# Kernel tuning notes

Measured on AMD Instinct MI355X. Metric: run time of the kernel, lower is better.

## Reference

```python
import jax, jax.numpy as jnp
import numpy as np

B, N, FIN = 512, 256, 32   # batch, num_agents, (tgt_feat+rbt_feat)*2
H1, G, FOUT, K, ACT = 16, 8, 16, 3, 5  # compress dims, shared feat G, GF out, taps, actions


def setup_inputs() -> dict:
    key = jax.random.key(0)
    ks = jax.random.split(key, 10)
    x = jax.random.normal(ks[0], (B, N, FIN), dtype=jnp.float32)
    # GSO, scaled ~1/sqrt(N) so repeated shifts stay numerically tame
    S = jax.random.normal(ks[1], (B, N, N), dtype=jnp.float32) * (1.0 / np.sqrt(N))
    def lin(k, fout, fin):
        return jax.random.normal(k, (fout, fin), dtype=jnp.float32) * (1.0 / np.sqrt(fin))
    W1, b1 = lin(ks[2], H1, FIN), jnp.zeros((H1,), jnp.float32)
    W2, b2 = lin(ks[3], G, H1), jnp.zeros((G,), jnp.float32)
    # graph-filter taps: [FOUT, K, G] (E=1 folded away)
    Hgf = jax.random.normal(ks[4], (FOUT, K, G), dtype=jnp.float32) * (1.0 / np.sqrt(K * G))
    bgf = jnp.zeros((FOUT,), jnp.float32)
    Wa, ba = lin(ks[5], ACT, FOUT), jnp.zeros((ACT,), jnp.float32)
    return {"x": x, "S": S, "W1": W1, "b1": b1, "W2": W2, "b2": b2,
            "Hgf": Hgf, "bgf": bgf, "Wa": Wa, "ba": ba}


def reference(x, S, W1, b1, W2, b2, Hgf, bgf, Wa, ba):
    # compress MLP, batched over all agents at once (replaces the per-agent loop)
    h = jax.nn.relu(jnp.einsum('bnf,hf->bnh', x, W1) + b1)
    h = jax.nn.relu(jnp.einsum('bnh,gh->bng', h, W2) + b2)   # [B, N, G]
    z = jnp.transpose(h, (0, 2, 1))                          # [B, G, N]
    # K-tap graph shift: z_k = z_{k-1} @ S
    taps = [z]
    for _ in range(K - 1):
        taps.append(jnp.einsum('bgn,bnm->bgm', taps[-1], S))
    zK = jnp.stack(taps, axis=1)                             # [B, K, G, N]
    y = jnp.einsum('fkg,bkgn->bfn', Hgf, zK) + bgf[None, :, None]
    y = jax.nn.relu(y)                                       # [B, FOUT, N]
    # action MLP per agent (single linear, batched over agents)
    actions = jnp.einsum('bfn,af->bna', y, Wa) + ba          # [B, N, ACT]
    return actions
```

## Files before the change

kernel.cpp:

```cpp
#include <hip/hip_runtime.h>

constexpr int Bsz  = 512;
constexpr int Nn   = 256;
constexpr int FINc = 32;
constexpr int H1c  = 16;
constexpr int Gc   = 8;
constexpr int FOUTc= 16;
constexpr int Kc   = 3;
constexpr int ACTc = 5;

__global__ __launch_bounds__(512, 4)
void cpn_kernel(const float* __restrict__ x,  const float* __restrict__ S,
                const float* __restrict__ W1, const float* __restrict__ b1,
                const float* __restrict__ W2, const float* __restrict__ b2,
                const float* __restrict__ Hgf,const float* __restrict__ bgf,
                const float* __restrict__ Wa, const float* __restrict__ ba,
                float* __restrict__ out)
{
    const int b    = blockIdx.x;
    const int tid  = threadIdx.x;
    const int wid  = tid >> 6;
    const int lane = tid & 63;
    const int rg   = wid >> 1;
    const int cg   = wid & 1;
    const int n    = tid;

    __shared__ __align__(16) float zA[Nn][Gc];
    __shared__ __align__(16) float zB[Nn][Gc];
    __shared__ __align__(16) float zpart[4][Gc][Nn];

    float z0r[Gc];
    if (tid < Nn) {
        float xr[FINc];
        const float4* xp = reinterpret_cast<const float4*>(x + ((size_t)b * Nn + n) * FINc);
        #pragma unroll
        for (int i = 0; i < FINc / 4; ++i) {
            float4 v = xp[i];
            xr[4*i+0] = v.x; xr[4*i+1] = v.y; xr[4*i+2] = v.z; xr[4*i+3] = v.w;
        }
        float h1v[H1c];
        #pragma unroll
        for (int h = 0; h < H1c; ++h) {
            float a = b1[h];
            #pragma unroll
            for (int f = 0; f < FINc; ++f) a = fmaf(W1[h*FINc + f], xr[f], a);
            h1v[h] = fmaxf(a, 0.0f);
        }
        #pragma unroll
        for (int g = 0; g < Gc; ++g) {
            float a = b2[g];
            #pragma unroll
            for (int h = 0; h < H1c; ++h) a = fmaf(W2[g*H1c + h], h1v[h], a);
            z0r[g] = fmaxf(a, 0.0f);
            zA[n][g] = z0r[g];
        }
    }
    __syncthreads();

    float z1r[Gc], z2r[Gc];

    auto spass = [&](const float (*zsrc)[Gc], float* zred) {
        float acc[Gc][2];
        #pragma unroll
        for (int g = 0; g < Gc; ++g) { acc[g][0] = 0.0f; acc[g][1] = 0.0f; }

        const float* srow = S + ((size_t)b * Nn + rg * 64) * Nn + cg * 128 + 2 * lane;
        #pragma unroll 16
        for (int i = 0; i < 64; ++i) {
            const float2 sv = *reinterpret_cast<const float2*>(srow);
            srow += Nn;
            const int nn = rg * 64 + i;
            const float4 za = *reinterpret_cast<const float4*>(&zsrc[nn][0]);
            const float4 zb = *reinterpret_cast<const float4*>(&zsrc[nn][4]);
            const float zg[Gc] = {za.x, za.y, za.z, za.w, zb.x, zb.y, zb.z, zb.w};
            #pragma unroll
            for (int g = 0; g < Gc; ++g) {
                acc[g][0] = fmaf(zg[g], sv.x, acc[g][0]);
                acc[g][1] = fmaf(zg[g], sv.y, acc[g][1]);
            }
        }
        #pragma unroll
        for (int g = 0; g < Gc; ++g) {
            *reinterpret_cast<float2*>(&zpart[rg][g][cg * 128 + 2 * lane]) =
                make_float2(acc[g][0], acc[g][1]);
        }
        __syncthreads();
        if (tid < Nn) {
            #pragma unroll
            for (int g = 0; g < Gc; ++g)
                zred[g] = (zpart[0][g][n] + zpart[1][g][n]) + (zpart[2][g][n] + zpart[3][g][n]);
        }
    };

    spass(zA, z1r);
    if (tid < Nn) {
        #pragma unroll
        for (int g = 0; g < Gc; ++g) zB[n][g] = z1r[g];
    }
    __syncthreads();
    spass(zB, z2r);

    if (tid < Nn) {
        float y[FOUTc];
        #pragma unroll
        for (int f = 0; f < FOUTc; ++f) y[f] = bgf[f];
        #pragma unroll
        for (int g = 0; g < Gc; ++g) {
            const float zv = z0r[g];
            #pragma unroll
            for (int f = 0; f < FOUTc; ++f) y[f] = fmaf(Hgf[f*(Kc*Gc) + 0*Gc + g], zv, y[f]);
        }
        #pragma unroll
        for (int g = 0; g < Gc; ++g) {
            const float zv = z1r[g];
            #pragma unroll
            for (int f = 0; f < FOUTc; ++f) y[f] = fmaf(Hgf[f*(Kc*Gc) + 1*Gc + g], zv, y[f]);
        }
        #pragma unroll
        for (int g = 0; g < Gc; ++g) {
            const float zv = z2r[g];
            #pragma unroll
            for (int f = 0; f < FOUTc; ++f) y[f] = fmaf(Hgf[f*(Kc*Gc) + 2*Gc + g], zv, y[f]);
        }
        #pragma unroll
        for (int f = 0; f < FOUTc; ++f) y[f] = fmaxf(y[f], 0.0f);

        float* op = out + ((size_t)b * Nn + n) * ACTc;
        #pragma unroll
        for (int a = 0; a < ACTc; ++a) {
            float acc = ba[a];
            #pragma unroll
            for (int f = 0; f < FOUTc; ++f) acc = fmaf(Wa[a*FOUTc + f], y[f], acc);
            op[a] = acc;
        }
    }
}

extern "C" void kernel_launch(void* const* d_in, const int* in_sizes, int n_in,
                              void* d_out, int out_size, void* d_ws, size_t ws_size,
                              hipStream_t stream) {
    const float* x   = (const float*)d_in[0];
    const float* S   = (const float*)d_in[1];
    const float* W1  = (const float*)d_in[2];
    const float* b1  = (const float*)d_in[3];
    const float* W2  = (const float*)d_in[4];
    const float* b2  = (const float*)d_in[5];
    const float* Hgf = (const float*)d_in[6];
    const float* bgf = (const float*)d_in[7];
    const float* Wa  = (const float*)d_in[8];
    const float* ba  = (const float*)d_in[9];

    cpn_kernel<<<dim3(Bsz), dim3(512), 0, stream>>>(
        x, S, W1, b1, W2, b2, Hgf, bgf, Wa, ba, (float*)d_out);
}
```

Before: 52.21 us.

## Repartition S pass into 32-row warp slabs with float4 loads and register double-buffering

Each wavefront now covers 32 rows of S across all 256 columns, reading float4 values per lane instead of float2 over half the columns. S rows are prefetched eight at a time into a register double buffer. Partial sums are combined in two stages through shared memory, and z0/z1 are re-read from LDS rather than held in registers, which eases register pressure. The larger accumulator tile (8x4) and the prefetch buffers add registers, which may reduce occupancy under the 512x4 launch bound.

```diff
diff --git a/kernel.cpp b/kernel.cpp
--- a/kernel.cpp
+++ b/kernel.cpp
@@ -21,15 +21,12 @@
     const int tid  = threadIdx.x;
     const int wid  = tid >> 6;
     const int lane = tid & 63;
-    const int rg   = wid >> 1;
-    const int cg   = wid & 1;
     const int n    = tid;
 
     __shared__ __align__(16) float zA[Nn][Gc];
     __shared__ __align__(16) float zB[Nn][Gc];
     __shared__ __align__(16) float zpart[4][Gc][Nn];
 
-    float z0r[Gc];
     if (tid < Nn) {
         float xr[FINc];
         const float4* xp = reinterpret_cast<const float4*>(x + ((size_t)b * Nn + n) * FINc);
@@ -51,8 +48,7 @@
             float a = b2[g];
             #pragma unroll
             for (int h = 0; h < H1c; ++h) a = fmaf(W2[g*H1c + h], h1v[h], a);
-            z0r[g] = fmaxf(a, 0.0f);
-            zA[n][g] = z0r[g];
+            zA[n][g] = fmaxf(a, 0.0f);
         }
     }
     __syncthreads();
@@ -60,29 +56,58 @@
     float z1r[Gc], z2r[Gc];
 
     auto spass = [&](const float (*zsrc)[Gc], float* zred) {
-        float acc[Gc][2];
+        float acc[Gc][4];
         #pragma unroll
-        for (int g = 0; g < Gc; ++g) { acc[g][0] = 0.0f; acc[g][1] = 0.0f; }
+        for (int g = 0; g < Gc; ++g)
+            #pragma unroll
+            for (int j = 0; j < 4; ++j) acc[g][j] = 0.0f;
 
-        const float* srow = S + ((size_t)b * Nn + rg * 64) * Nn + cg * 128 + 2 * lane;
-        #pragma unroll 16
-        for (int i = 0; i < 64; ++i) {
-            const float2 sv = *reinterpret_cast<const float2*>(srow);
-            srow += Nn;
-            const int nn = rg * 64 + i;
-            const float4 za = *reinterpret_cast<const float4*>(&zsrc[nn][0]);
-            const float4 zb = *reinterpret_cast<const float4*>(&zsrc[nn][4]);
-            const float zg[Gc] = {za.x, za.y, za.z, za.w, zb.x, zb.y, zb.z, zb.w};
+        const float* sbase = S + ((size_t)b * Nn + wid * 32) * Nn + 4 * lane;
+
+        float4 buf[8], nbuf[8];
+        #pragma unroll
+        for (int i = 0; i < 8; ++i) buf[i] = *reinterpret_cast<const float4*>(sbase + (size_t)i * Nn);
+        #pragma unroll
+        for (int c = 0; c < 4; ++c) {
+            if (c < 3) {
+                #pragma unroll
+                for (int i = 0; i < 8; ++i)
+                    nbuf[i] = *reinterpret_cast<const float4*>(sbase + (size_t)((c + 1) * 8 + i) * Nn);
+            }
+            #pragma unroll
+            for (int i = 0; i < 8; ++i) {
+                const int nn = wid * 32 + c * 8 + i;
+                const float4 za = *reinterpret_cast<const float4*>(&zsrc[nn][0]);
+                const float4 zb = *reinterpret_cast<const float4*>(&zsrc[nn][4]);
+                const float zg[Gc] = {za.x, za.y, za.z, za.w, zb.x, zb.y, zb.z, zb.w};
+                #pragma unroll
+                for (int g = 0; g < Gc; ++g) {
+                    acc[g][0] = fmaf(zg[g], buf[i].x, acc[g][0]);
+                    acc[g][1] = fmaf(zg[g], buf[i].y, acc[g][1]);
+                    acc[g][2] = fmaf(zg[g], buf[i].z, acc[g][2]);
+                    acc[g][3] = fmaf(zg[g], buf[i].w, acc[g][3]);
+                }
+            }
+            if (c < 3) {
+                #pragma unroll
+                for (int i = 0; i < 8; ++i) buf[i] = nbuf[i];
+            }
+        }
+
+        if (wid < 4) {
+            #pragma unroll
+            for (int g = 0; g < Gc; ++g)
+                *reinterpret_cast<float4*>(&zpart[wid][g][4 * lane]) =
+                    make_float4(acc[g][0], acc[g][1], acc[g][2], acc[g][3]);
+        }
+        __syncthreads();
+        if (wid >= 4) {
             #pragma unroll
             for (int g = 0; g < Gc; ++g) {
-                acc[g][0] = fmaf(zg[g], sv.x, acc[g][0]);
-                acc[g][1] = fmaf(zg[g], sv.y, acc[g][1]);
+                float4 cur = *reinterpret_cast<const float4*>(&zpart[wid - 4][g][4 * lane]);
+                cur.x += acc[g][0]; cur.y += acc[g][1]; cur.z += acc[g][2]; cur.w += acc[g][3];
+                *reinterpret_cast<float4*>(&zpart[wid - 4][g][4 * lane]) = cur;
             }
-        }
-        #pragma unroll
-        for (int g = 0; g < Gc; ++g) {
-            *reinterpret_cast<float2*>(&zpart[rg][g][cg * 128 + 2 * lane]) =
-                make_float2(acc[g][0], acc[g][1]);
         }
         __syncthreads();
         if (tid < Nn) {
@@ -101,26 +126,30 @@
     spass(zB, z2r);
 
     if (tid < Nn) {
+        const float4 a0 = *reinterpret_cast<const float4*>(&zA[n][0]);
+        const float4 a1 = *reinterpret_cast<const float4*>(&zA[n][4]);
+        const float4 b0 = *reinterpret_cast<const float4*>(&zB[n][0]);
+        const float4 b1v= *reinterpret_cast<const float4*>(&zB[n][4]);
+        const float z0g[Gc] = {a0.x, a0.y, a0.z, a0.w, a1.x, a1.y, a1.z, a1.w};
+        const float z1g[Gc] = {b0.x, b0.y, b0.z, b0.w, b1v.x, b1v.y, b1v.z, b1v.w};
+
         float y[FOUTc];
         #pragma unroll
         for (int f = 0; f < FOUTc; ++f) y[f] = bgf[f];
         #pragma unroll
         for (int g = 0; g < Gc; ++g) {
-            const float zv = z0r[g];
             #pragma unroll
-            for (int f = 0; f < FOUTc; ++f) y[f] = fmaf(Hgf[f*(Kc*Gc) + 0*Gc + g], zv, y[f]);
+            for (int f = 0; f < FOUTc; ++f) y[f] = fmaf(Hgf[f*(Kc*Gc) + 0*Gc + g], z0g[g], y[f]);
         }
         #pragma unroll
         for (int g = 0; g < Gc; ++g) {
-            const float zv = z1r[g];
             #pragma unroll
-            for (int f = 0; f < FOUTc; ++f) y[f] = fmaf(Hgf[f*(Kc*Gc) + 1*Gc + g], zv, y[f]);
+            for (int f = 0; f < FOUTc; ++f) y[f] = fmaf(Hgf[f*(Kc*Gc) + 1*Gc + g], z1g[g], y[f]);
         }
         #pragma unroll
         for (int g = 0; g < Gc; ++g) {
-            const float zv = z2r[g];
             #pragma unroll
-            for (int f = 0; f < FOUTc; ++f) y[f] = fmaf(Hgf[f*(Kc*Gc) + 2*Gc + g], zv, y[f]);
+            for (int f = 0; f < FOUTc; ++f) y[f] = fmaf(Hgf[f*(Kc*Gc) + 2*Gc + g], z2r[g], y[f]);
         }
         #pragma unroll
         for (int f = 0; f < FOUTc; ++f) y[f] = fmaxf(y[f], 0.0f);
```

Measured after the change: 67.16 us. 1.29x slower.

## Double block size to 1024 threads and store partial sums in half precision

Applied to the files above, without the earlier changes.

The block grows to 1024 threads, so each of 16 wavefronts handles 32 rows of S instead of 64, and the S-shift work is split 8 ways across row groups. Partial sums go into shared memory as fp16 to keep the larger zpart buffer small, and they are reduced in a separate merge step. z0 and z1 are read back from shared memory rather than held in registers, and the first MLP is reordered to stream x directly. The aim is more memory parallelism for the S reads and lower register pressure. The cost is fp16 rounding error in the graph-shift results, and launch_bounds(1024, 8) may force register spills.

```diff
diff --git a/kernel.cpp b/kernel.cpp
--- a/kernel.cpp
+++ b/kernel.cpp
@@ -1,4 +1,5 @@
 #include <hip/hip_runtime.h>
+#include <hip/hip_fp16.h>
 
 constexpr int Bsz  = 512;
 constexpr int Nn   = 256;
@@ -9,7 +10,7 @@
 constexpr int Kc   = 3;
 constexpr int ACTc = 5;
 
-__global__ __launch_bounds__(512, 4)
+__global__ __launch_bounds__(1024, 8)
 void cpn_kernel(const float* __restrict__ x,  const float* __restrict__ S,
                 const float* __restrict__ W1, const float* __restrict__ b1,
                 const float* __restrict__ W2, const float* __restrict__ b2,
@@ -25,51 +26,49 @@
     const int cg   = wid & 1;
     const int n    = tid;
 
-    __shared__ __align__(16) float zA[Nn][Gc];
-    __shared__ __align__(16) float zB[Nn][Gc];
-    __shared__ __align__(16) float zpart[4][Gc][Nn];
+    __shared__ __align__(16) float  zA[Nn][Gc];
+    __shared__ __align__(16) float  zB[Nn][Gc];
+    __shared__ __align__(16) __half zpart[8][Gc][Nn];
 
-    float z0r[Gc];
     if (tid < Nn) {
-        float xr[FINc];
         const float4* xp = reinterpret_cast<const float4*>(x + ((size_t)b * Nn + n) * FINc);
+        float h1v[H1c];
+        #pragma unroll
+        for (int h = 0; h < H1c; ++h) h1v[h] = b1[h];
         #pragma unroll
         for (int i = 0; i < FINc / 4; ++i) {
-            float4 v = xp[i];
-            xr[4*i+0] = v.x; xr[4*i+1] = v.y; xr[4*i+2] = v.z; xr[4*i+3] = v.w;
+            const float4 v = xp[i];
+            #pragma unroll
+            for (int h = 0; h < H1c; ++h) {
+                h1v[h] = fmaf(W1[h*FINc + 4*i+0], v.x, h1v[h]);
+                h1v[h] = fmaf(W1[h*FINc + 4*i+1], v.y, h1v[h]);
+                h1v[h] = fmaf(W1[h*FINc + 4*i+2], v.z, h1v[h]);
+                h1v[h] = fmaf(W1[h*FINc + 4*i+3], v.w, h1v[h]);
+            }
         }
-        float h1v[H1c];
         #pragma unroll
-        for (int h = 0; h < H1c; ++h) {
-            float a = b1[h];
-            #pragma unroll
-            for (int f = 0; f < FINc; ++f) a = fmaf(W1[h*FINc + f], xr[f], a);
-            h1v[h] = fmaxf(a, 0.0f);
-        }
+        for (int h = 0; h < H1c; ++h) h1v[h] = fmaxf(h1v[h], 0.0f);
         #pragma unroll
         for (int g = 0; g < Gc; ++g) {
             float a = b2[g];
             #pragma unroll
             for (int h = 0; h < H1c; ++h) a = fmaf(W2[g*H1c + h], h1v[h], a);
-            z0r[g] = fmaxf(a, 0.0f);
-            zA[n][g] = z0r[g];
+            zA[n][g] = fmaxf(a, 0.0f);
         }
     }
     __syncthreads();
 
-    float z1r[Gc], z2r[Gc];
-
-    auto spass = [&](const float (*zsrc)[Gc], float* zred) {
+    auto spass = [&](const float (*zsrc)[Gc]) {
         float acc[Gc][2];
         #pragma unroll
         for (int g = 0; g < Gc; ++g) { acc[g][0] = 0.0f; acc[g][1] = 0.0f; }
 
-        const float* srow = S + ((size_t)b * Nn + rg * 64) * Nn + cg * 128 + 2 * lane;
-        #pragma unroll 16
-        for (int i = 0; i < 64; ++i) {
+        const float* srow = S + ((size_t)b * Nn + rg * 32) * Nn + cg * 128 + 2 * lane;
+        #pragma unroll
+        for (int i = 0; i < 32; ++i) {
             const float2 sv = *reinterpret_cast<const float2*>(srow);
             srow += Nn;
-            const int nn = rg * 64 + i;
+            const int nn = rg * 32 + i;
             const float4 za = *reinterpret_cast<const float4*>(&zsrc[nn][0]);
             const float4 zb = *reinterpret_cast<const float4*>(&zsrc[nn][4]);
             const float zg[Gc] = {za.x, za.y, za.z, za.w, zb.x, zb.y, zb.z, zb.w};
@@ -81,46 +80,61 @@
         }
         #pragma unroll
         for (int g = 0; g < Gc; ++g) {
-            *reinterpret_cast<float2*>(&zpart[rg][g][cg * 128 + 2 * lane]) =
-                make_float2(acc[g][0], acc[g][1]);
-        }
-        __syncthreads();
-        if (tid < Nn) {
-            #pragma unroll
-            for (int g = 0; g < Gc; ++g)
-                zred[g] = (zpart[0][g][n] + zpart[1][g][n]) + (zpart[2][g][n] + zpart[3][g][n]);
+            *reinterpret_cast<__half2*>(&zpart[rg][g][cg * 128 + 2 * lane]) =
+                __float22half2_rn(make_float2(acc[g][0], acc[g][1]));
         }
     };
 
-    spass(zA, z1r);
+    auto merge = [&](float* zr) {
+        #pragma unroll
+        for (int g = 0; g < Gc; ++g) {
+            float a = 0.0f;
+            #pragma unroll
+            for (int r = 0; r < 8; ++r) a += __half2float(zpart[r][g][n]);
+            zr[g] = a;
+        }
+    };
+
+    spass(zA);
+    __syncthreads();
     if (tid < Nn) {
+        float z1r[Gc];
+        merge(z1r);
         #pragma unroll
         for (int g = 0; g < Gc; ++g) zB[n][g] = z1r[g];
     }
     __syncthreads();
-    spass(zB, z2r);
+    spass(zB);
+    __syncthreads();
 
     if (tid < Nn) {
+        float z2r[Gc];
+        merge(z2r);
+
+        const float4 a0 = *reinterpret_cast<const float4*>(&zA[n][0]);
+        const float4 a1 = *reinterpret_cast<const float4*>(&zA[n][4]);
+        const float4 c0 = *reinterpret_cast<const float4*>(&zB[n][0]);
+        const float4 c1 = *reinterpret_cast<const float4*>(&zB[n][4]);
+        const float z0g[Gc] = {a0.x, a0.y, a0.z, a0.w, a1.x, a1.y, a1.z, a1.w};
+        const float z1g[Gc] = {c0.x, c0.y, c0.z, c0.w, c1.x, c1.y, c1.z, c1.w};
+
         float y[FOUTc];
         #pragma unroll
         for (int f = 0; f < FOUTc; ++f) y[f] = bgf[f];
         #pragma unroll
         for (int g = 0; g < Gc; ++g) {
-            const float zv = z0r[g];
             #pragma unroll
-            for (int f = 0; f < FOUTc; ++f) y[f] = fmaf(Hgf[f*(Kc*Gc) + 0*Gc + g], zv, y[f]);
+            for (int f = 0; f < FOUTc; ++f) y[f] = fmaf(Hgf[f*(Kc*Gc) + 0*Gc + g], z0g[g], y[f]);
         }
         #pragma unroll
         for (int g = 0; g < Gc; ++g) {
-            const float zv = z1r[g];
             #pragma unroll
-            for (int f = 0; f < FOUTc; ++f) y[f] = fmaf(Hgf[f*(Kc*Gc) + 1*Gc + g], zv, y[f]);
+            for (int f = 0; f < FOUTc; ++f) y[f] = fmaf(Hgf[f*(Kc*Gc) + 1*Gc + g], z1g[g], y[f]);
         }
         #pragma unroll
         for (int g = 0; g < Gc; ++g) {
-            const float zv = z2r[g];
             #pragma unroll
-            for (int f = 0; f < FOUTc; ++f) y[f] = fmaf(Hgf[f*(Kc*Gc) + 2*Gc + g], zv, y[f]);
+            for (int f = 0; f < FOUTc; ++f) y[f] = fmaf(Hgf[f*(Kc*Gc) + 2*Gc + g], z2r[g], y[f]);
         }
         #pragma unroll
         for (int f = 0; f < FOUTc; ++f) y[f] = fmaxf(y[f], 0.0f);
@@ -150,6 +164,6 @@
     const float* Wa  = (const float*)d_in[8];
     const float* ba  = (const float*)d_in[9];
 
-    cpn_kernel<<<dim3(Bsz), dim3(512), 0, stream>>>(
+    cpn_kernel<<<dim3(Bsz), dim3(1024), 0, stream>>>(
         x, S, W1, b1, W2, b2, Hgf, bgf, Wa, ba, (float*)d_out);
 }
```

Measured after the change: 82.47 us. 57.9% more time.
